# Kernel optimization log

Hardware: AMD Instinct MI355X
Metric: run time of the kernel (lower is better)

## Reference

```python
import jax, jax.numpy as jnp
import numpy as np

N = 50000
E = 800000
F_IN, H1, H2, C = 512, 256, 32, 16


def _glorot(key, shape):
    lim = float(np.sqrt(6.0 / (shape[0] + shape[1])))
    return jax.random.uniform(key, shape, jnp.float32, -lim, lim)


def setup_inputs() -> dict:
    key = jax.random.key(0)
    ks = jax.random.split(key, 8)
    x = jax.random.normal(ks[0], (N, F_IN), jnp.float32)
    edge_index = jax.random.randint(ks[1], (2, E), 0, N, jnp.int64)
    return {
        "x": x,
        "edge_index": edge_index,
        "W1": _glorot(ks[2], (F_IN, H1)), "b1": jnp.zeros((H1,), jnp.float32),
        "W2": _glorot(ks[3], (H1, H2)), "b2": jnp.zeros((H2,), jnp.float32),
        "W3": _glorot(ks[4], (H2, C)), "b3": jnp.zeros((C,), jnp.float32),
    }


def _gcn_norm(edge_index, n_nodes):
    # Add self-loops, compute symmetric normalization deg^-1/2[src]*deg^-1/2[dst]
    loop = jnp.arange(n_nodes, dtype=edge_index.dtype)
    src = jnp.concatenate([edge_index[0], loop])
    dst = jnp.concatenate([edge_index[1], loop])
    ones = jnp.ones(src.shape[0], jnp.float32)
    deg = jax.ops.segment_sum(ones, dst, num_segments=n_nodes)
    dinv = jnp.where(deg > 0, jax.lax.rsqrt(deg), 0.0)
    norm = dinv[src] * dinv[dst]  # [E+N]
    return src, dst, norm


def _gcn_conv(x, W, b, src, dst, norm, n_nodes):
    h = x @ W  # transform first (reduces scatter width)
    msg = h[src] * norm[:, None]  # gather + scale, [E+N, out]
    out = jax.ops.segment_sum(msg, dst, num_segments=n_nodes)
    return out + b


def reference(x, edge_index, W1, b1, W2, b2, W3, b3):
    n_nodes = x.shape[0]
    src, dst, norm = _gcn_norm(edge_index, n_nodes)
    h = _gcn_conv(x, W1, b1, src, dst, norm, n_nodes)
    h = jax.nn.relu(h)  # dropout is identity in eval mode
    h = _gcn_conv(h, W2, b2, src, dst, norm, n_nodes)
    h = jax.nn.relu(h)
    h = _gcn_conv(h, W3, b3, src, dst, norm, n_nodes)
    return h
```

## Files before the change

kernel.cpp:

```cpp
#include <hip/hip_runtime.h>

constexpr int N   = 50000;
constexpr int E   = 800000;
constexpr int FIN = 512;
constexpr int H1v = 256;
constexpr int H2v = 32;
constexpr int Cv  = 16;

constexpr int NBLK = (N + 1023) / 1024;

typedef __attribute__((ext_vector_type(8))) short short8;
typedef __attribute__((ext_vector_type(4))) float f32x4;
typedef __attribute__((ext_vector_type(4))) unsigned short us4;
typedef __attribute__((ext_vector_type(8))) unsigned short us8;
typedef __attribute__((ext_vector_type(4))) unsigned int uint4v;

__device__ inline unsigned short f2bf(float f) {
    unsigned u = __float_as_uint(f);
    return (unsigned short)((u + 0x7FFFu + ((u >> 16) & 1u)) >> 16);
}
__device__ inline float bf2f(unsigned short b) { return __uint_as_float(((unsigned)b) << 16); }


__global__ __launch_bounds__(256) void k_init(const float* __restrict__ W,
                                              unsigned short* __restrict__ Wf,
                                              int* __restrict__ cnt) {
    const int b = blockIdx.x;
    if (b < 64) {
        int t = b * 256 + threadIdx.x;
        int l = t & 63, nt = (t >> 6) & 15, kt = t >> 10;
        int n = nt * 16 + (l & 15);
        int kb = kt * 32 + (l >> 4) * 8;
        short8 h8, l8;
#pragma unroll
        for (int j = 0; j < 8; ++j) {
            float w = W[(size_t)(kb + j) * H1v + n];
            unsigned short h = f2bf(w);
            h8[j] = (short)h;
            l8[j] = (short)f2bf(w - bf2f(h));
        }
        size_t base = ((size_t)(kt * 16 + nt) * 2) * 512 + (size_t)l * 8;
        *(short8*)(Wf + base) = h8;
        *(short8*)(Wf + base + 512) = l8;
    } else {
        int i = (b - 64) * 256 + threadIdx.x;
        if (i <= N) cnt[i] = 0;
    }
}


__global__ __launch_bounds__(256) void k_hist(const int* __restrict__ dst,
                                              int* __restrict__ cnt) {
    int e = blockIdx.x * 256 + threadIdx.x;
    if (e < E) atomicAdd(&cnt[dst[e]], 1);
}

__global__ __launch_bounds__(256) void k_scan_part(const int* __restrict__ cnt,
                                                   int* __restrict__ bsum) {
    __shared__ int red[256];
    const int t = threadIdx.x;
    const int base = blockIdx.x * 1024 + t * 4;
    int s = 0;
#pragma unroll
    for (int i = 0; i < 4; ++i) {
        int idx = base + i;
        if (idx < N) s += cnt[idx];
    }
    red[t] = s;
    __syncthreads();
    for (int off = 128; off > 0; off >>= 1) {
        if (t < off) red[t] += red[t + off];
        __syncthreads();
    }
    if (t == 0) bsum[blockIdx.x] = red[0];
}

__global__ __launch_bounds__(256) void k_scan_final(const int* __restrict__ cnt,
                                                    const int* __restrict__ bsum,
                                                    int* __restrict__ row_ptr,
                                                    int* __restrict__ cursor,
                                                    float* __restrict__ dinv) {
    __shared__ int sums[256];
    __shared__ int s_bofs, s_tot;
    const int t = threadIdx.x;

    if (t < 64) {
        int v = (t < NBLK) ? bsum[t] : 0;
        int pre = (t < (int)blockIdx.x) ? v : 0;
#pragma unroll
        for (int off = 32; off > 0; off >>= 1) {
            pre += __shfl_down(pre, off, 64);
            v   += __shfl_down(v, off, 64);
        }
        if (t == 0) { s_bofs = pre; s_tot = v; }
    }

    const int base = blockIdx.x * 1024 + t * 4;
    int v[4];
    int local = 0;
#pragma unroll
    for (int i = 0; i < 4; ++i) {
        int idx = base + i;
        v[i] = (idx < N) ? cnt[idx] : 0;
        local += v[i];
    }
    sums[t] = local;
    __syncthreads();
    for (int off = 1; off < 256; off <<= 1) {
        int u = (t >= off) ? sums[t - off] : 0;
        __syncthreads();
        sums[t] += u;
        __syncthreads();
    }
    int run = s_bofs + sums[t] - local;
#pragma unroll
    for (int i = 0; i < 4; ++i) {
        int idx = base + i;
        if (idx < N) {
            row_ptr[idx] = run;
            cursor[idx] = run;
            dinv[idx] = rsqrtf(1.0f + (float)v[i]);
        }
        run += v[i];
    }
    if (blockIdx.x == NBLK - 1 && t == 0) row_ptr[N] = s_tot;
}

__global__ __launch_bounds__(256) void k_permute(const int* __restrict__ src,
                                                 const int* __restrict__ dst,
                                                 int* __restrict__ cursor,
                                                 int* __restrict__ srcs) {
    int e = blockIdx.x * 256 + threadIdx.x;
    if (e < E) {
        int pos = atomicAdd(&cursor[dst[e]], 1);
        srcs[pos] = src[e];
    }
}


__device__ inline void split_pair(float x0, float x1, unsigned& hp, unsigned& lp) {
    unsigned u0 = __float_as_uint(x0), u1 = __float_as_uint(x1);
    unsigned h0 = u0 & 0xffff0000u, h1 = u1 & 0xffff0000u;
    float l0 = x0 - __uint_as_float(h0);
    float l1 = x1 - __uint_as_float(h1);
    hp = __builtin_amdgcn_perm(u1, u0, 0x07060302u);
    lp = __builtin_amdgcn_perm(__float_as_uint(l1), __float_as_uint(l0), 0x07060302u);
}

__device__ inline void split_frag(const float4& a, const float4& b, short8& hi, short8& lo) {
    unsigned h0, h1, h2, h3, l0, l1, l2, l3;
    split_pair(a.x, a.y, h0, l0);
    split_pair(a.z, a.w, h1, l1);
    split_pair(b.x, b.y, h2, l2);
    split_pair(b.z, b.w, h3, l3);
    uint4v h, l;
    h[0] = h0; h[1] = h1; h[2] = h2; h[3] = h3;
    l[0] = l0; l[1] = l1; l[2] = l2; l[3] = l3;
    hi = __builtin_bit_cast(short8, h);
    lo = __builtin_bit_cast(short8, l);
}

__device__ inline void stage_x_tile(const float* __restrict__ X, int brow, int k0,
                                    float* lds, int tid) {
    const int wbase = tid & ~63;
#pragma unroll
    for (int c = 0; c < 4; ++c) {
        int q = c * 256 + tid;
        int row = q >> 4;
        int gc = ((q & 15) ^ (row & 15)) << 2;
        int r = brow + row;
        const float* src = X + (size_t)(r < N ? r : 0) * FIN + k0 + gc;
        float* dst = lds + (size_t)(c * 256 + wbase) * 4;
        __builtin_amdgcn_global_load_lds((const __attribute__((address_space(1))) void*)src,
                                         (__attribute__((address_space(3))) void*)dst,
                                         16, 0, 0);
    }
}

__global__ __launch_bounds__(256, 4) void k_gemm1_mfma(const float* __restrict__ X,
                                                       const unsigned short* __restrict__ Wf,
                                                       const float* __restrict__ dinv,
                                                       unsigned short* __restrict__ Hout) {
    __shared__ float As[2][4096];
    const int tid = threadIdx.x;
    const int w = tid >> 6, l = tid & 63;
    const int wr = w >> 1, wc = w & 1;
    const int brow = blockIdx.x * 64;
    const int row0 = brow + wr * 32;
    const int wrow = wr * 32;
    const int colb = blockIdx.y;
    const int lm = l & 15;
    const int lk2 = (l >> 4) * 2;

    const unsigned short* bp0 = Wf + (size_t)(colb * 8 + wc * 4) * 1024 + (size_t)l * 8;

    f32x4 acc[2][4];
#pragma unroll
    for (int i = 0; i < 2; ++i)
#pragma unroll
        for (int j = 0; j < 4; ++j) acc[i][j] = (f32x4)0.f;

    stage_x_tile(X, brow, 0, As[0], tid);

    for (int kt = 0; kt < 8; ++kt) {
        const int cur = kt & 1;
        __syncthreads();

        const unsigned short* bpA = bp0 + (size_t)(2 * kt) * 16384;
        short8 B0h[4], B0l[4];
#pragma unroll
        for (int j = 0; j < 4; ++j) {
            B0h[j] = *(const short8*)(bpA + j * 1024);
            B0l[j] = *(const short8*)(bpA + j * 1024 + 512);
        }

        if (kt < 7) stage_x_tile(X, brow, (kt + 1) * 64, As[cur ^ 1], tid);

        const float* Ab = As[cur];

        short8 Ah[2], Al[2];
#pragma unroll
        for (int i = 0; i < 2; ++i) {
            int row = wrow + i * 16 + lm;
            const float* rbp = Ab + row * 64;
            int p = row & 15;
            float4 a0 = *(const float4*)(rbp + ((lk2 ^ p) << 2));
            float4 a1 = *(const float4*)(rbp + (((lk2 + 1) ^ p) << 2));
            split_frag(a0, a1, Ah[i], Al[i]);
        }

        const unsigned short* bpB = bpA + 16384;
        short8 B1h[4], B1l[4];
#pragma unroll
        for (int j = 0; j < 4; ++j) {
            B1h[j] = *(const short8*)(bpB + j * 1024);
            B1l[j] = *(const short8*)(bpB + j * 1024 + 512);
        }

#pragma unroll
        for (int i = 0; i < 2; ++i)
#pragma unroll
            for (int j = 0; j < 4; ++j) {
                acc[i][j] = __builtin_amdgcn_mfma_f32_16x16x32_bf16(Ah[i], B0h[j], acc[i][j], 0, 0, 0);
                acc[i][j] = __builtin_amdgcn_mfma_f32_16x16x32_bf16(Ah[i], B0l[j], acc[i][j], 0, 0, 0);
                acc[i][j] = __builtin_amdgcn_mfma_f32_16x16x32_bf16(Al[i], B0h[j], acc[i][j], 0, 0, 0);
            }

#pragma unroll
        for (int i = 0; i < 2; ++i) {
            int row = wrow + i * 16 + lm;
            const float* rbp = Ab + row * 64;
            int p = row & 15;
            int g0 = lk2 + 8;
            float4 a0 = *(const float4*)(rbp + ((g0 ^ p) << 2));
            float4 a1 = *(const float4*)(rbp + (((g0 + 1) ^ p) << 2));
            split_frag(a0, a1, Ah[i], Al[i]);
        }

#pragma unroll
        for (int i = 0; i < 2; ++i)
#pragma unroll
            for (int j = 0; j < 4; ++j) {
                acc[i][j] = __builtin_amdgcn_mfma_f32_16x16x32_bf16(Ah[i], B1h[j], acc[i][j], 0, 0, 0);
                acc[i][j] = __builtin_amdgcn_mfma_f32_16x16x32_bf16(Ah[i], B1l[j], acc[i][j], 0, 0, 0);
                acc[i][j] = __builtin_amdgcn_mfma_f32_16x16x32_bf16(Al[i], B1h[j], acc[i][j], 0, 0, 0);
            }
    }

    const int col0 = colb * 128 + wc * 64;
#pragma unroll
    for (int i = 0; i < 2; ++i) {
        int rbase = row0 + i * 16 + (l >> 4) * 4;
        float dv[4];
        bool okr[4];
#pragma unroll
        for (int r = 0; r < 4; ++r) {
            int rr = rbase + r;
            okr[r] = rr < N;
            dv[r] = okr[r] ? dinv[rr] : 0.f;
        }
#pragma unroll
        for (int j = 0; j < 4; ++j) {
            int col = col0 + j * 16 + lm;
#pragma unroll
            for (int r = 0; r < 4; ++r)
                if (okr[r]) Hout[(size_t)(rbase + r) * H1v + col] = f2bf(acc[i][j][r] * dv[r]);
        }
    }
}


__global__ __launch_bounds__(256) void k_gemm2(const float* __restrict__ A,
                                               const float* __restrict__ W,
                                               const float* __restrict__ dinv,
                                               unsigned short* __restrict__ Hout) {
    __shared__ float Ws[H1v * H2v];
    const int tid = threadIdx.x;
#pragma unroll
    for (int i = 0; i < 8; ++i) {
        int off = tid * 4 + i * 1024;
        *(float4*)(&Ws[off]) = *(const float4*)(W + off);
    }
    __syncthreads();

    const int row = blockIdx.x * 8 + (tid >> 5);
    const int col = tid & 31;
    if (row >= N) return;
    const float* arow = A + (size_t)row * H1v;
    float sum = 0.f;
#pragma unroll 4
    for (int k = 0; k < H1v; k += 4) {
        float4 a4 = *(const float4*)(arow + k);
        sum = fmaf(a4.x, Ws[(k + 0) * H2v + col], sum);
        sum = fmaf(a4.y, Ws[(k + 1) * H2v + col], sum);
        sum = fmaf(a4.z, Ws[(k + 2) * H2v + col], sum);
        sum = fmaf(a4.w, Ws[(k + 3) * H2v + col], sum);
    }
    Hout[(size_t)row * H2v + col] = f2bf(sum * dinv[row]);
}


__global__ __launch_bounds__(256) void k_agg_d256(const unsigned short* __restrict__ h,
                                                  const int* __restrict__ rp,
                                                  const int* __restrict__ srcs,
                                                  const float* __restrict__ dinv,
                                                  const float* __restrict__ bias,
                                                  float* __restrict__ out) {
    const int half = threadIdx.x >> 5;
    const int lane = threadIdx.x & 31;
    const int d = blockIdx.x * 8 + half;
    if (d >= N) return;
    const int beg = rp[d], end = rp[d + 1];
    const int fo = lane * 8;
    const unsigned short* hb = h + fo;
    us8 sv = *(const us8*)(hb + (size_t)d * H1v);
    float a[8];
#pragma unroll
    for (int q = 0; q < 8; ++q) a[q] = bf2f(sv[q]);
    int j = beg;
    for (; j + 3 < end; j += 4) {
        int s0 = srcs[j], s1 = srcs[j + 1], s2 = srcs[j + 2], s3 = srcs[j + 3];
        us8 v0 = *(const us8*)(hb + (size_t)s0 * H1v);
        us8 v1 = *(const us8*)(hb + (size_t)s1 * H1v);
        us8 v2 = *(const us8*)(hb + (size_t)s2 * H1v);
        us8 v3 = *(const us8*)(hb + (size_t)s3 * H1v);
#pragma unroll
        for (int q = 0; q < 8; ++q)
            a[q] += bf2f(v0[q]) + bf2f(v1[q]) + bf2f(v2[q]) + bf2f(v3[q]);
    }
    for (; j < end; ++j) {
        us8 v = *(const us8*)(hb + (size_t)srcs[j] * H1v);
#pragma unroll
        for (int q = 0; q < 8; ++q) a[q] += bf2f(v[q]);
    }
    const float di = dinv[d];
    const float4 b0 = *(const float4*)(bias + fo);
    const float4 b1 = *(const float4*)(bias + fo + 4);
    float4 o0, o1;
    o0.x = fmaxf(fmaf(di, a[0], b0.x), 0.f);
    o0.y = fmaxf(fmaf(di, a[1], b0.y), 0.f);
    o0.z = fmaxf(fmaf(di, a[2], b0.z), 0.f);
    o0.w = fmaxf(fmaf(di, a[3], b0.w), 0.f);
    o1.x = fmaxf(fmaf(di, a[4], b1.x), 0.f);
    o1.y = fmaxf(fmaf(di, a[5], b1.y), 0.f);
    o1.z = fmaxf(fmaf(di, a[6], b1.z), 0.f);
    o1.w = fmaxf(fmaf(di, a[7], b1.w), 0.f);
    *(float4*)(out + (size_t)d * H1v + fo) = o0;
    *(float4*)(out + (size_t)d * H1v + fo + 4) = o1;
}


__global__ __launch_bounds__(256) void k_agg32_gemm3(const unsigned short* __restrict__ h2,
                                                     const int* __restrict__ rp,
                                                     const int* __restrict__ srcs,
                                                     const float* __restrict__ dinv,
                                                     const float* __restrict__ b2,
                                                     const float* __restrict__ W3,
                                                     unsigned short* __restrict__ h3) {
    __shared__ float als[16][33];
    __shared__ float W3s[H2v * Cv];
    const int t = threadIdx.x;
    *(float2*)(&W3s[t * 2]) = *(const float2*)(W3 + t * 2);

    const int sub = t >> 4, fg = t & 15;
    const int d = blockIdx.x * 16 + sub;
    const int beg = rp[d], end = rp[d + 1];
    const unsigned short* h2b = h2 + fg * 2;
    unsigned sv = *(const unsigned*)(h2b + (size_t)d * H2v);
    float a0 = __uint_as_float(sv << 16);
    float a1 = __uint_as_float(sv & 0xffff0000u);
    int j = beg;
    for (; j + 3 < end; j += 4) {
        unsigned v0 = *(const unsigned*)(h2b + (size_t)srcs[j] * H2v);
        unsigned v1 = *(const unsigned*)(h2b + (size_t)srcs[j + 1] * H2v);
        unsigned v2 = *(const unsigned*)(h2b + (size_t)srcs[j + 2] * H2v);
        unsigned v3 = *(const unsigned*)(h2b + (size_t)srcs[j + 3] * H2v);
        a0 += __uint_as_float(v0 << 16) + __uint_as_float(v1 << 16)
            + __uint_as_float(v2 << 16) + __uint_as_float(v3 << 16);
        a1 += __uint_as_float(v0 & 0xffff0000u) + __uint_as_float(v1 & 0xffff0000u)
            + __uint_as_float(v2 & 0xffff0000u) + __uint_as_float(v3 & 0xffff0000u);
    }
    for (; j < end; ++j) {
        unsigned v = *(const unsigned*)(h2b + (size_t)srcs[j] * H2v);
        a0 += __uint_as_float(v << 16);
        a1 += __uint_as_float(v & 0xffff0000u);
    }
    const float di = dinv[d];
    als[sub][fg * 2]     = fmaxf(fmaf(di, a0, b2[fg * 2]), 0.f);
    als[sub][fg * 2 + 1] = fmaxf(fmaf(di, a1, b2[fg * 2 + 1]), 0.f);
    __syncthreads();

    const int row = t >> 4, col = t & 15;
    float sum = 0.f;
#pragma unroll
    for (int k = 0; k < H2v; ++k) sum = fmaf(als[row][k], W3s[k * Cv + col], sum);
    const int gr = blockIdx.x * 16 + row;
    h3[(size_t)gr * Cv + col] = f2bf(sum * dinv[gr]);
}


__global__ __launch_bounds__(256) void k_agg16(const unsigned short* __restrict__ h,
                                               const int* __restrict__ rp,
                                               const int* __restrict__ srcs,
                                               const float* __restrict__ dinv,
                                               const float* __restrict__ bias,
                                               float* __restrict__ out) {
    const int sub = threadIdx.x >> 3;
    const int fg = threadIdx.x & 7;
    const int d = blockIdx.x * 32 + sub;
    if (d >= N) return;
    const int beg = rp[d], end = rp[d + 1];
    const unsigned short* hb = h + fg * 2;
    unsigned sv = *(const unsigned*)(hb + (size_t)d * Cv);
    float a0 = __uint_as_float(sv << 16);
    float a1 = __uint_as_float(sv & 0xffff0000u);
    int j = beg;
    for (; j + 3 < end; j += 4) {
        unsigned v0 = *(const unsigned*)(hb + (size_t)srcs[j] * Cv);
        unsigned v1 = *(const unsigned*)(hb + (size_t)srcs[j + 1] * Cv);
        unsigned v2 = *(const unsigned*)(hb + (size_t)srcs[j + 2] * Cv);
        unsigned v3 = *(const unsigned*)(hb + (size_t)srcs[j + 3] * Cv);
        a0 += __uint_as_float(v0 << 16) + __uint_as_float(v1 << 16)
            + __uint_as_float(v2 << 16) + __uint_as_float(v3 << 16);
        a1 += __uint_as_float(v0 & 0xffff0000u) + __uint_as_float(v1 & 0xffff0000u)
            + __uint_as_float(v2 & 0xffff0000u) + __uint_as_float(v3 & 0xffff0000u);
    }
    for (; j < end; ++j) {
        unsigned v = *(const unsigned*)(hb + (size_t)srcs[j] * Cv);
        a0 += __uint_as_float(v << 16);
        a1 += __uint_as_float(v & 0xffff0000u);
    }
    const float di = dinv[d];
    float2 o;
    o.x = fmaf(di, a0, bias[fg * 2]);
    o.y = fmaf(di, a1, bias[fg * 2 + 1]);
    *(float2*)(out + (size_t)d * Cv + fg * 2) = o;
}


extern "C" void kernel_launch(void* const* d_in, const int* in_sizes, int n_in,
                              void* d_out, int out_size, void* d_ws, size_t ws_size,
                              hipStream_t stream) {
    const float* x  = (const float*)d_in[0];
    const int*   ei = (const int*)d_in[1];
    const float* W1 = (const float*)d_in[2];
    const float* b1 = (const float*)d_in[3];
    const float* W2 = (const float*)d_in[4];
    const float* b2 = (const float*)d_in[5];
    const float* W3 = (const float*)d_in[6];
    const float* b3 = (const float*)d_in[7];
    const int* src = ei;
    const int* dst = ei + E;
    float* out = (float*)d_out;

    char* ws = (char*)d_ws;
    float* dinv   = (float*)ws;
    int*   cnt    = (int*)(ws + 0x40000);
    int*   rp     = cnt;
    int*   cursor = (int*)(ws + 0x80000);
    int*   bsum   = (int*)(ws + 0xB2000);
    int*   srcs   = (int*)(ws + 0xC0000);
    unsigned short* wsplit = (unsigned short*)(ws + (size_t)4 * 1024 * 1024);
    char* p = ws + (size_t)5 * 1024 * 1024;
    unsigned short* h1 = (unsigned short*)p; p += (size_t)N * H1v * sizeof(unsigned short);
    float*          a1 = (float*)p;          p += (size_t)N * H1v * sizeof(float);
    unsigned short* h2 = (unsigned short*)p; p += (size_t)N * H2v * sizeof(unsigned short);
    unsigned short* h3 = (unsigned short*)p;

    k_init<<<64 + (N + 256) / 256, 256, 0, stream>>>(W1, wsplit, cnt);
    k_hist<<<(E + 255) / 256, 256, 0, stream>>>(dst, cnt);
    k_scan_part<<<NBLK, 256, 0, stream>>>(cnt, bsum);
    k_scan_final<<<NBLK, 256, 0, stream>>>(cnt, bsum, rp, cursor, dinv);
    k_permute<<<(E + 255) / 256, 256, 0, stream>>>(src, dst, cursor, srcs);

    dim3 g1((N + 63) / 64, 2);
    k_gemm1_mfma<<<g1, 256, 0, stream>>>(x, wsplit, dinv, h1);
    k_agg_d256<<<(N + 7) / 8, 256, 0, stream>>>(h1, rp, srcs, dinv, b1, a1);

    k_gemm2<<<N / 8, 256, 0, stream>>>(a1, W2, dinv, h2);

    k_agg32_gemm3<<<N / 16, 256, 0, stream>>>(h2, rp, srcs, dinv, b2, W3, h3);

    k_agg16<<<(N + 31) / 32, 256, 0, stream>>>(h3, rp, srcs, dinv, b3, out);
}
```

Measured before the change: 425.9 us.

## Fuse layer-1 aggregation with layer-2 GEMM through shared memory

Merges the 256-wide neighbour aggregation and the 256x32 projection into one kernel: each block aggregates 8 destination rows into LDS, then multiplies them by W2 held in shared memory. This removes the N x 256 fp32 intermediate write and re-read plus one launch. It also unrolls the gather loop to 8 neighbours for more memory-level parallelism. The cost is 40KB of LDS per block, which may limit occupancy.

```diff
diff --git a/kernel.cpp b/kernel.cpp
--- a/kernel.cpp
+++ b/kernel.cpp
@@ -39,7 +39,7 @@
             h8[j] = (short)h;
             l8[j] = (short)f2bf(w - bf2f(h));
         }
-        size_t base = ((size_t)(kt * 16 + nt) * 2) * 512 + (size_t)l * 8;
+        size_t base = (size_t)(kt * 16 + nt) * 1024 + (size_t)l * 8;
         *(short8*)(Wf + base) = h8;
         *(short8*)(Wf + base + 512) = l8;
     } else {
@@ -290,46 +290,25 @@
 }
 
 
-__global__ __launch_bounds__(256) void k_gemm2(const float* __restrict__ A,
-                                               const float* __restrict__ W,
-                                               const float* __restrict__ dinv,
-                                               unsigned short* __restrict__ Hout) {
-    __shared__ float Ws[H1v * H2v];
-    const int tid = threadIdx.x;
+__global__ __launch_bounds__(256, 4) void k_agg_gemm2(const unsigned short* __restrict__ h,
+                                                      const int* __restrict__ rp,
+                                                      const int* __restrict__ srcs,
+                                                      const float* __restrict__ dinv,
+                                                      const float* __restrict__ bias,
+                                                      const float* __restrict__ W2,
+                                                      unsigned short* __restrict__ h2) {
+    __shared__ float als[8][256];
+    __shared__ float W2s[H1v * H2v];
+    const int t = threadIdx.x;
 #pragma unroll
     for (int i = 0; i < 8; ++i) {
-        int off = tid * 4 + i * 1024;
-        *(float4*)(&Ws[off]) = *(const float4*)(W + off);
-    }
-    __syncthreads();
-
-    const int row = blockIdx.x * 8 + (tid >> 5);
-    const int col = tid & 31;
-    if (row >= N) return;
-    const float* arow = A + (size_t)row * H1v;
-    float sum = 0.f;
-#pragma unroll 4
-    for (int k = 0; k < H1v; k += 4) {
-        float4 a4 = *(const float4*)(arow + k);
-        sum = fmaf(a4.x, Ws[(k + 0) * H2v + col], sum);
-        sum = fmaf(a4.y, Ws[(k + 1) * H2v + col], sum);
-        sum = fmaf(a4.z, Ws[(k + 2) * H2v + col], sum);
-        sum = fmaf(a4.w, Ws[(k + 3) * H2v + col], sum);
-    }
-    Hout[(size_t)row * H2v + col] = f2bf(sum * dinv[row]);
-}
-
-
-__global__ __launch_bounds__(256) void k_agg_d256(const unsigned short* __restrict__ h,
-                                                  const int* __restrict__ rp,
-                                                  const int* __restrict__ srcs,
-                                                  const float* __restrict__ dinv,
-                                                  const float* __restrict__ bias,
-                                                  float* __restrict__ out) {
-    const int half = threadIdx.x >> 5;
-    const int lane = threadIdx.x & 31;
+        int off = t * 4 + i * 1024;
+        *(float4*)(&W2s[off]) = *(const float4*)(W2 + off);
+    }
+
+    const int half = t >> 5;
+    const int lane = t & 31;
     const int d = blockIdx.x * 8 + half;
-    if (d >= N) return;
     const int beg = rp[d], end = rp[d + 1];
     const int fo = lane * 8;
     const unsigned short* hb = h + fo;
@@ -338,12 +317,25 @@
 #pragma unroll
     for (int q = 0; q < 8; ++q) a[q] = bf2f(sv[q]);
     int j = beg;
+    for (; j + 7 < end; j += 8) {
+        us8 v0 = *(const us8*)(hb + (size_t)srcs[j] * H1v);
+        us8 v1 = *(const us8*)(hb + (size_t)srcs[j + 1] * H1v);
+        us8 v2 = *(const us8*)(hb + (size_t)srcs[j + 2] * H1v);
+        us8 v3 = *(const us8*)(hb + (size_t)srcs[j + 3] * H1v);
+        us8 v4 = *(const us8*)(hb + (size_t)srcs[j + 4] * H1v);
+        us8 v5 = *(const us8*)(hb + (size_t)srcs[j + 5] * H1v);
+        us8 v6 = *(const us8*)(hb + (size_t)srcs[j + 6] * H1v);
+        us8 v7 = *(const us8*)(hb + (size_t)srcs[j + 7] * H1v);
+#pragma unroll
+        for (int q = 0; q < 8; ++q)
+            a[q] += ((bf2f(v0[q]) + bf2f(v1[q])) + (bf2f(v2[q]) + bf2f(v3[q])))
+                  + ((bf2f(v4[q]) + bf2f(v5[q])) + (bf2f(v6[q]) + bf2f(v7[q])));
+    }
     for (; j + 3 < end; j += 4) {
-        int s0 = srcs[j], s1 = srcs[j + 1], s2 = srcs[j + 2], s3 = srcs[j + 3];
-        us8 v0 = *(const us8*)(hb + (size_t)s0 * H1v);
-        us8 v1 = *(const us8*)(hb + (size_t)s1 * H1v);
-        us8 v2 = *(const us8*)(hb + (size_t)s2 * H1v);
-        us8 v3 = *(const us8*)(hb + (size_t)s3 * H1v);
+        us8 v0 = *(const us8*)(hb + (size_t)srcs[j] * H1v);
+        us8 v1 = *(const us8*)(hb + (size_t)srcs[j + 1] * H1v);
+        us8 v2 = *(const us8*)(hb + (size_t)srcs[j + 2] * H1v);
+        us8 v3 = *(const us8*)(hb + (size_t)srcs[j + 3] * H1v);
 #pragma unroll
         for (int q = 0; q < 8; ++q)
             a[q] += bf2f(v0[q]) + bf2f(v1[q]) + bf2f(v2[q]) + bf2f(v3[q]);
@@ -356,17 +348,26 @@
     const float di = dinv[d];
     const float4 b0 = *(const float4*)(bias + fo);
     const float4 b1 = *(const float4*)(bias + fo + 4);
-    float4 o0, o1;
-    o0.x = fmaxf(fmaf(di, a[0], b0.x), 0.f);
-    o0.y = fmaxf(fmaf(di, a[1], b0.y), 0.f);
-    o0.z = fmaxf(fmaf(di, a[2], b0.z), 0.f);
-    o0.w = fmaxf(fmaf(di, a[3], b0.w), 0.f);
-    o1.x = fmaxf(fmaf(di, a[4], b1.x), 0.f);
-    o1.y = fmaxf(fmaf(di, a[5], b1.y), 0.f);
-    o1.z = fmaxf(fmaf(di, a[6], b1.z), 0.f);
-    o1.w = fmaxf(fmaf(di, a[7], b1.w), 0.f);
-    *(float4*)(out + (size_t)d * H1v + fo) = o0;
-    *(float4*)(out + (size_t)d * H1v + fo + 4) = o1;
+    als[half][fo + 0] = fmaxf(fmaf(di, a[0], b0.x), 0.f);
+    als[half][fo + 1] = fmaxf(fmaf(di, a[1], b0.y), 0.f);
+    als[half][fo + 2] = fmaxf(fmaf(di, a[2], b0.z), 0.f);
+    als[half][fo + 3] = fmaxf(fmaf(di, a[3], b0.w), 0.f);
+    als[half][fo + 4] = fmaxf(fmaf(di, a[4], b1.x), 0.f);
+    als[half][fo + 5] = fmaxf(fmaf(di, a[5], b1.y), 0.f);
+    als[half][fo + 6] = fmaxf(fmaf(di, a[6], b1.z), 0.f);
+    als[half][fo + 7] = fmaxf(fmaf(di, a[7], b1.w), 0.f);
+    __syncthreads();
+
+    float sum = 0.f;
+#pragma unroll 8
+    for (int k = 0; k < H1v; k += 4) {
+        float4 av = *(const float4*)(&als[half][k]);
+        sum = fmaf(av.x, W2s[(k + 0) * H2v + lane], sum);
+        sum = fmaf(av.y, W2s[(k + 1) * H2v + lane], sum);
+        sum = fmaf(av.z, W2s[(k + 2) * H2v + lane], sum);
+        sum = fmaf(av.w, W2s[(k + 3) * H2v + lane], sum);
+    }
+    h2[(size_t)d * H2v + lane] = f2bf(sum * di);
 }
 
 
@@ -483,7 +484,6 @@
     unsigned short* wsplit = (unsigned short*)(ws + (size_t)4 * 1024 * 1024);
     char* p = ws + (size_t)5 * 1024 * 1024;
     unsigned short* h1 = (unsigned short*)p; p += (size_t)N * H1v * sizeof(unsigned short);
-    float*          a1 = (float*)p;          p += (size_t)N * H1v * sizeof(float);
     unsigned short* h2 = (unsigned short*)p; p += (size_t)N * H2v * sizeof(unsigned short);
     unsigned short* h3 = (unsigned short*)p;
 
@@ -495,9 +495,8 @@
 
     dim3 g1((N + 63) / 64, 2);
     k_gemm1_mfma<<<g1, 256, 0, stream>>>(x, wsplit, dinv, h1);
-    k_agg_d256<<<(N + 7) / 8, 256, 0, stream>>>(h1, rp, srcs, dinv, b1, a1);
-
-    k_gemm2<<<N / 8, 256, 0, stream>>>(a1, W2, dinv, h2);
+
+    k_agg_gemm2<<<N / 8, 256, 0, stream>>>(h1, rp, srcs, dinv, b1, W2, h2);
 
     k_agg32_gemm3<<<N / 16, 256, 0, stream>>>(h2, rp, srcs, dinv, b2, W3, h3);
 
```

Result: faster. 394.1 us (-7.5%).
